# Optimization experiments

Hardware: AMD Instinct MI355X
Metric: run time of the kernel (lower is better)

Reference implementation:

```python
import jax, jax.numpy as jnp
import numpy as np

DIM = 1024
NPATCH = 256
NWINDOW = 8
HEADS = 16
DIM_HEAD = 64
T = NPATCH * NWINDOW  # 2048
B = 4


def setup_inputs() -> dict:
    key = jax.random.key(0)
    k1, k2, k3 = jax.random.split(key, 3)
    inner = HEADS * DIM_HEAD
    return {
        "x": jax.random.normal(k1, (B, T, DIM), dtype=jnp.float32),
        "ln_gamma": jnp.ones((DIM,), jnp.float32),
        "ln_beta": jnp.zeros((DIM,), jnp.float32),
        "w_qkv": jax.random.normal(k2, (DIM, 3 * inner), dtype=jnp.float32) * (DIM ** -0.5),
        "w_out": jax.random.normal(k3, (inner, DIM), dtype=jnp.float32) * (inner ** -0.5),
        "b_out": jnp.zeros((DIM,), jnp.float32),
    }


def reference(x, ln_gamma, ln_beta, w_qkv, w_out, b_out):
    Bq, Tq, C = x.shape
    # LayerNorm over last dim (eps matches torch default 1e-5)
    mu = jnp.mean(x, axis=-1, keepdims=True)
    var = jnp.mean(jnp.square(x - mu), axis=-1, keepdims=True)
    xn = (x - mu) * jax.lax.rsqrt(var + 1e-5) * ln_gamma + ln_beta
    # QKV projection (no bias), split heads: b t (h d) -> b h t d
    qkv = xn @ w_qkv  # [B, T, 3*H*D]
    q, k, v = jnp.split(qkv, 3, axis=-1)
    split_heads = lambda t: t.reshape(Bq, Tq, HEADS, DIM_HEAD).transpose(0, 2, 1, 3)
    q, k, v = split_heads(q), split_heads(k), split_heads(v)
    scale = DIM_HEAD ** -0.5
    dots = jnp.einsum("bhqd,bhkd->bhqk", q, k) * scale  # [B, H, T, T]
    # Block-causal mask: key block index <= query block index (block size = NPATCH)
    blk = jnp.arange(Tq) // NPATCH
    mask = blk[:, None] >= blk[None, :]  # [T, T] bool
    dots = jnp.where(mask, dots, jnp.float32(-jnp.inf))
    attn = jax.nn.softmax(dots, axis=-1)
    out = jnp.einsum("bhqk,bhkd->bhqd", attn, v)
    out = out.transpose(0, 2, 1, 3).reshape(Bq, Tq, HEADS * DIM_HEAD)
    return out @ w_out + b_out
```

## Files before the change

### kernel.cpp

```cpp
#include <hip/hip_runtime.h>
#include <hip/hip_bf16.h>
#include <stdint.h>

#define H_HEADS 16
#define D_HEAD  64
#define T_SEQ   2048
#define N_B     4
#define DIM_    1024
#define M_TOT   8192
#define N_QKV   3072

typedef unsigned short u16;
using f32x4  = __attribute__((ext_vector_type(4))) float;
using f32x16 = __attribute__((ext_vector_type(16))) float;
using bf16x8 = __attribute__((ext_vector_type(8))) short;

typedef __attribute__((address_space(3))) unsigned int lds_u32;
typedef __attribute__((address_space(1))) unsigned int glb_u32;

__device__ __forceinline__ void gload16(const u16* g, u16* l) {
  __builtin_amdgcn_global_load_lds((const glb_u32*)g, (lds_u32*)l, 16, 0, 0);
}

__device__ __forceinline__ u16 f2b(float f) {
  unsigned u = __builtin_bit_cast(unsigned, f);
  u += 0x7fffu + ((u >> 16) & 1u);
  return (u16)(u >> 16);
}

__global__ __launch_bounds__(256) void ln_kernel(const float* __restrict__ x,
    const float* __restrict__ gam, const float* __restrict__ bet,
    u16* __restrict__ xn)
{
  int row = blockIdx.x;
  int t = threadIdx.x;
  const float4* xr = (const float4*)(x + (size_t)row * DIM_);
  float4 v = xr[t];
  float s  = v.x + v.y + v.z + v.w;
  float s2 = v.x * v.x + v.y * v.y + v.z * v.z + v.w * v.w;
#pragma unroll
  for (int o = 32; o > 0; o >>= 1) { s += __shfl_down(s, o); s2 += __shfl_down(s2, o); }
  __shared__ float rs[4], rq[4];
  int w = t >> 6;
  if ((t & 63) == 0) { rs[w] = s; rq[w] = s2; }
  __syncthreads();
  float S  = rs[0] + rs[1] + rs[2] + rs[3];
  float S2 = rq[0] + rq[1] + rq[2] + rq[3];
  float mu   = S * (1.0f / DIM_);
  float var  = S2 * (1.0f / DIM_) - mu * mu;
  float rstd = rsqrtf(var + 1e-5f);
  float4 g4 = ((const float4*)gam)[t];
  float4 b4 = ((const float4*)bet)[t];
  ushort4 o;
  o.x = f2b((v.x - mu) * rstd * g4.x + b4.x);
  o.y = f2b((v.y - mu) * rstd * g4.y + b4.y);
  o.z = f2b((v.z - mu) * rstd * g4.z + b4.z);
  o.w = f2b((v.w - mu) * rstd * g4.w + b4.w);
  ((ushort4*)(xn + (size_t)row * DIM_))[t] = o;
}

__global__ __launch_bounds__(256) void transpose_cvt(const float* __restrict__ src,
    u16* __restrict__ dst, int K, int N)
{
  __shared__ u16 tile[32][33];
  int n0 = blockIdx.x * 32, k0 = blockIdx.y * 32;
  int tx = threadIdx.x, ty = threadIdx.y;
#pragma unroll
  for (int i = 0; i < 4; ++i) {
    int k = k0 + ty + i * 8;
    tile[tx][ty + i * 8] = f2b(src[(size_t)k * N + n0 + tx]);
  }
  __syncthreads();
#pragma unroll
  for (int i = 0; i < 4; ++i) {
    int n = n0 + ty + i * 8;
    dst[(size_t)n * K + k0 + tx] = tile[ty + i * 8][tx];
  }
}

template<int EPI>
__global__ __launch_bounds__(256) void gemm_bt(
    const u16* __restrict__ A, const u16* __restrict__ Bt, int K,
    u16* __restrict__ Qb, u16* __restrict__ Kb, u16* __restrict__ Vt,
    const float* __restrict__ bias, float* __restrict__ outF)
{
  __shared__ __align__(16) u16 lA[128 * 32];
  __shared__ __align__(16) u16 lB[128 * 32];
  int tid = threadIdx.x;
  int bn = blockIdx.x * 128, bm = blockIdx.y * 128;
  int lane = tid & 63, w = tid >> 6;
  int wr = w >> 1, wc = w & 1;
  int g = lane >> 4, r16 = lane & 15;
  const f32x4 fzero = {0.f, 0.f, 0.f, 0.f};
  f32x4 acc[4][4];
#pragma unroll
  for (int i = 0; i < 4; ++i)
#pragma unroll
    for (int j = 0; j < 4; ++j) acc[i][j] = fzero;

  const u16* Ab = A + (size_t)bm * K;
  const u16* Bb = Bt + (size_t)bn * K;

  for (int kt = 0; kt < K; kt += 32) {
    __syncthreads();
#pragma unroll
    for (int it = 0; it < 2; ++it) {
      int c = tid + it * 256;
      int row = c >> 2;
      int sc = (c & 3) ^ (row & 3);
      gload16(Ab + (size_t)row * K + kt + sc * 8, lA + c * 8);
      gload16(Bb + (size_t)row * K + kt + sc * 8, lB + c * 8);
    }
    __syncthreads();
    bf16x8 af[4], bf[4];
#pragma unroll
    for (int i = 0; i < 4; ++i) {
      int rl = wr * 64 + i * 16 + r16;
      af[i] = *(const bf16x8*)(lA + rl * 32 + ((g ^ (rl & 3)) << 3));
    }
#pragma unroll
    for (int j = 0; j < 4; ++j) {
      int rl = wc * 64 + j * 16 + r16;
      bf[j] = *(const bf16x8*)(lB + rl * 32 + ((g ^ (rl & 3)) << 3));
    }
#pragma unroll
    for (int i = 0; i < 4; ++i)
#pragma unroll
      for (int j = 0; j < 4; ++j)
        acc[i][j] = __builtin_amdgcn_mfma_f32_16x16x32_bf16(af[i], bf[j], acc[i][j], 0, 0, 0);
  }

  if (EPI == 0) {
    int part = bn >> 10;
#pragma unroll
    for (int i = 0; i < 4; ++i) {
#pragma unroll
      for (int j = 0; j < 4; ++j) {
        int n = bn + wc * 64 + j * 16 + r16;
        int nn = n & 1023;
        int h = nn >> 6, d = nn & 63;
#pragma unroll
        for (int rr = 0; rr < 4; ++rr) {
          int m = bm + wr * 64 + i * 16 + g * 4 + rr;
          int b = m >> 11, t = m & 2047;
          size_t bh = (size_t)(b * H_HEADS + h);
          float vv = acc[i][j][rr];
          if (part == 0)      Qb[(bh * T_SEQ + t) * D_HEAD + d] = f2b(vv * 0.18033688f);
          else if (part == 1) Kb[(bh * T_SEQ + t) * D_HEAD + d] = f2b(vv);
          else                Vt[(bh * D_HEAD + d) * T_SEQ + t] = f2b(vv);
        }
      }
    }
  } else {
#pragma unroll
    for (int i = 0; i < 4; ++i) {
#pragma unroll
      for (int j = 0; j < 4; ++j) {
        int n = bn + wc * 64 + j * 16 + r16;
        float bb = bias[n];
#pragma unroll
        for (int rr = 0; rr < 4; ++rr) {
          int m = bm + wr * 64 + i * 16 + g * 4 + rr;
          outF[(size_t)m * DIM_ + n] = acc[i][j][rr] + bb;
        }
      }
    }
  }
}

__global__ __launch_bounds__(512, 4) void attn_kernel(
    const u16* __restrict__ Qb, const u16* __restrict__ Kb,
    const u16* __restrict__ Vt, u16* __restrict__ AO)
{
  __shared__ __align__(16) u16 lK[2][64 * 64];
  __shared__ __align__(16) u16 lV[2][64 * 64];
  int bid = blockIdx.x;
  int bh6 = bid & 63;
  int h = bh6 & 15, b = bh6 >> 4;
  const int PERM[8] = {7, 5, 3, 1, 0, 2, 4, 6};
  int qt = PERM[bid >> 6];
  int nkt = (qt + 1) * 4;
  int tid = threadIdx.x, lane = tid & 63, w = tid >> 6;
  int q5 = lane & 31, hi = lane >> 5;
  size_t bh = (size_t)bh6;
  const u16* Qg = Qb + (bh * T_SEQ + (size_t)qt * 256) * D_HEAD;
  const u16* Kg = Kb + bh * T_SEQ * D_HEAD;
  const u16* Vg = Vt + bh * (size_t)D_HEAD * T_SEQ;

  bf16x8 qf[4];
#pragma unroll
  for (int kd = 0; kd < 4; ++kd)
    qf[kd] = *(const bf16x8*)(Qg + (w * 32 + q5) * D_HEAD + kd * 16 + hi * 8);

  f32x16 o0 = {0}, o1 = {0};
  float m_ = -1e30f, l_ = 0.f;

  auto STAGE = [&](int bs, int kt) {
    int c = tid;
    int row = c >> 3;
    int sc = (c & 7) ^ (row & 7);
    gload16(Kg + ((size_t)(kt * 64 + row)) * D_HEAD + sc * 8, &lK[bs][c * 8]);
    gload16(Vg + (size_t)row * T_SEQ + kt * 64 + sc * 8, &lV[bs][c * 8]);
  };

  STAGE(0, 0);
  int cur = 0;
  for (int kt = 0; kt < nkt; ++kt) {
    if (kt + 1 < nkt) {
      STAGE(cur ^ 1, kt + 1);
      asm volatile("s_waitcnt vmcnt(2)" ::: "memory");
    } else {
      asm volatile("s_waitcnt vmcnt(0)" ::: "memory");
    }
    __builtin_amdgcn_sched_barrier(0);
    __builtin_amdgcn_s_barrier();
    const u16* Kl = lK[cur];
    const u16* Vl = lV[cur];

    f32x16 s0 = {0}, s1 = {0};
    __builtin_amdgcn_s_setprio(1);
#pragma unroll
    for (int kd = 0; kd < 4; ++kd) {
      int ch = 2 * kd + hi;
      bf16x8 a0 = *(const bf16x8*)(Kl + q5 * 64 + ((ch ^ (q5 & 7)) << 3));
      bf16x8 a1 = *(const bf16x8*)(Kl + (32 + q5) * 64 + ((ch ^ (q5 & 7)) << 3));
      s0 = __builtin_amdgcn_mfma_f32_32x32x16_bf16(a0, qf[kd], s0, 0, 0, 0);
      s1 = __builtin_amdgcn_mfma_f32_32x32x16_bf16(a1, qf[kd], s1, 0, 0, 0);
    }
    __builtin_amdgcn_s_setprio(0);

    float pmax = fmaxf(s0[0], s1[0]);
#pragma unroll
    for (int r = 1; r < 16; ++r) pmax = fmaxf(pmax, fmaxf(s0[r], s1[r]));
    pmax = fmaxf(pmax, __shfl_xor(pmax, 32));
    float mnew = fmaxf(m_, pmax);
    float al = exp2f(m_ - mnew);
    m_ = mnew;
    float rsum = 0.f;
#pragma unroll
    for (int r = 0; r < 16; ++r) { s0[r] = exp2f(s0[r] - mnew); rsum += s0[r]; }
#pragma unroll
    for (int r = 0; r < 16; ++r) { s1[r] = exp2f(s1[r] - mnew); rsum += s1[r]; }
    rsum += __shfl_xor(rsum, 32);
    l_ = l_ * al + rsum;
    o0 *= al; o1 *= al;

    __builtin_amdgcn_s_setprio(1);
#pragma unroll
    for (int ks = 0; ks < 4; ++ks) {
      float v0 = (ks < 2) ? s0[(ks & 1) * 8 + 0] : s1[(ks & 1) * 8 + 0];
      float v1 = (ks < 2) ? s0[(ks & 1) * 8 + 1] : s1[(ks & 1) * 8 + 1];
      float v2 = (ks < 2) ? s0[(ks & 1) * 8 + 2] : s1[(ks & 1) * 8 + 2];
      float v3 = (ks < 2) ? s0[(ks & 1) * 8 + 3] : s1[(ks & 1) * 8 + 3];
      float v4 = (ks < 2) ? s0[(ks & 1) * 8 + 4] : s1[(ks & 1) * 8 + 4];
      float v5 = (ks < 2) ? s0[(ks & 1) * 8 + 5] : s1[(ks & 1) * 8 + 5];
      float v6 = (ks < 2) ? s0[(ks & 1) * 8 + 6] : s1[(ks & 1) * 8 + 6];
      float v7 = (ks < 2) ? s0[(ks & 1) * 8 + 7] : s1[(ks & 1) * 8 + 7];
      unsigned E0, E1, E2, E3;
      asm("v_cvt_pk_bf16_f32 %0, %1, %2" : "=v"(E0) : "v"(v0), "v"(v1));
      asm("v_cvt_pk_bf16_f32 %0, %1, %2" : "=v"(E1) : "v"(v2), "v"(v3));
      asm("v_cvt_pk_bf16_f32 %0, %1, %2" : "=v"(E2) : "v"(v4), "v"(v5));
      asm("v_cvt_pk_bf16_f32 %0, %1, %2" : "=v"(E3) : "v"(v6), "v"(v7));
      asm("v_permlane32_swap_b32 %0, %1" : "+v"(E0), "+v"(E2));
      asm("v_permlane32_swap_b32 %0, %1" : "+v"(E1), "+v"(E3));
      union { unsigned u[4]; bf16x8 v; } pk_;
      pk_.u[0] = E0; pk_.u[1] = E1; pk_.u[2] = E2; pk_.u[3] = E3;
      int ch = 2 * ks + hi;
      bf16x8 vf0 = *(const bf16x8*)(Vl + q5 * 64 + ((ch ^ (q5 & 7)) << 3));
      bf16x8 vf1 = *(const bf16x8*)(Vl + (32 + q5) * 64 + ((ch ^ (q5 & 7)) << 3));
      o0 = __builtin_amdgcn_mfma_f32_32x32x16_bf16(vf0, pk_.v, o0, 0, 0, 0);
      o1 = __builtin_amdgcn_mfma_f32_32x32x16_bf16(vf1, pk_.v, o1, 0, 0, 0);
    }
    __builtin_amdgcn_s_setprio(0);

    asm volatile("s_waitcnt lgkmcnt(0)" ::: "memory");
    __builtin_amdgcn_s_barrier();
    cur ^= 1;
  }

  float inv = 1.0f / l_;
  int t = qt * 256 + w * 32 + q5;
  u16* Ao = AO + ((size_t)b * T_SEQ + t) * DIM_ + h * 64;
#pragma unroll
  for (int rq = 0; rq < 4; ++rq) {
    ushort4 pk0, pk1;
    pk0.x = f2b(o0[rq * 4 + 0] * inv); pk0.y = f2b(o0[rq * 4 + 1] * inv);
    pk0.z = f2b(o0[rq * 4 + 2] * inv); pk0.w = f2b(o0[rq * 4 + 3] * inv);
    pk1.x = f2b(o1[rq * 4 + 0] * inv); pk1.y = f2b(o1[rq * 4 + 1] * inv);
    pk1.z = f2b(o1[rq * 4 + 2] * inv); pk1.w = f2b(o1[rq * 4 + 3] * inv);
    *(ushort4*)(Ao + rq * 8 + hi * 4)      = pk0;
    *(ushort4*)(Ao + 32 + rq * 8 + hi * 4) = pk1;
  }
}

extern "C" void kernel_launch(void* const* d_in, const int* in_sizes, int n_in,
                              void* d_out, int out_size, void* d_ws, size_t ws_size,
                              hipStream_t stream)
{
  const float* x    = (const float*)d_in[0];
  const float* gam  = (const float*)d_in[1];
  const float* bet  = (const float*)d_in[2];
  const float* wqkv = (const float*)d_in[3];
  const float* wout = (const float*)d_in[4];
  const float* bout = (const float*)d_in[5];
  float* out = (float*)d_out;

  u16* ws    = (u16*)d_ws;
  u16* xn    = ws;
  u16* wqkvT = xn    + (size_t)M_TOT * DIM_;
  u16* woutT = wqkvT + (size_t)N_QKV * DIM_;
  u16* Qb    = woutT + (size_t)DIM_ * DIM_;
  u16* Kb    = Qb    + (size_t)64 * T_SEQ * D_HEAD;
  u16* Vt    = Kb    + (size_t)64 * T_SEQ * D_HEAD;
  u16* AO    = xn;

  ln_kernel<<<M_TOT, 256, 0, stream>>>(x, gam, bet, xn);
  transpose_cvt<<<dim3(N_QKV / 32, DIM_ / 32), dim3(32, 8), 0, stream>>>(wqkv, wqkvT, DIM_, N_QKV);
  transpose_cvt<<<dim3(DIM_ / 32, DIM_ / 32), dim3(32, 8), 0, stream>>>(wout, woutT, DIM_, DIM_);
  gemm_bt<0><<<dim3(N_QKV / 128, M_TOT / 128), 256, 0, stream>>>(xn, wqkvT, DIM_, Qb, Kb, Vt, nullptr, nullptr);
  attn_kernel<<<N_B * H_HEADS * 8, 512, 0, stream>>>(Qb, Kb, Vt, AO);
  gemm_bt<1><<<dim3(DIM_ / 128, M_TOT / 128), 256, 0, stream>>>(AO, woutT, DIM_, nullptr, nullptr, nullptr, bout, out);
}
```

Baseline: 303.4 us.

## Rewrite projection GEMMs with 256x256 double-buffered tiles and 32x32 MFMA

Replaces the 128x128 single-buffered GEMM with a 512-thread kernel that computes 256x256 output tiles over a 64-wide K step. It uses 32x32x16 bf16 MFMA and double-buffers global-to-LDS loads so the next tile loads while the current one computes. It also maps blocks to XCDs for L2 locality and packs the V-transpose stores into 4-element vector writes. The aim is more data reuse per LDS byte and hidden load latency. In exchange, the 128KB LDS footprint allows only one block per CU, and the output projection launches just 128 blocks, which can leave CUs idle.

```diff
diff --git a/kernel.cpp b/kernel.cpp
--- a/kernel.cpp
+++ b/kernel.cpp
@@ -79,91 +79,137 @@
 }
 
 template<int EPI>
-__global__ __launch_bounds__(256) void gemm_bt(
-    const u16* __restrict__ A, const u16* __restrict__ Bt, int K,
+__global__ __launch_bounds__(512, 2) void gemm8(
+    const u16* __restrict__ A, const u16* __restrict__ Bt,
     u16* __restrict__ Qb, u16* __restrict__ Kb, u16* __restrict__ Vt,
     const float* __restrict__ bias, float* __restrict__ outF)
 {
-  __shared__ __align__(16) u16 lA[128 * 32];
-  __shared__ __align__(16) u16 lB[128 * 32];
-  int tid = threadIdx.x;
-  int bn = blockIdx.x * 128, bm = blockIdx.y * 128;
-  int lane = tid & 63, w = tid >> 6;
-  int wr = w >> 1, wc = w & 1;
-  int g = lane >> 4, r16 = lane & 15;
-  const f32x4 fzero = {0.f, 0.f, 0.f, 0.f};
-  f32x4 acc[4][4];
-#pragma unroll
-  for (int i = 0; i < 4; ++i)
-#pragma unroll
-    for (int j = 0; j < 4; ++j) acc[i][j] = fzero;
-
-  const u16* Ab = A + (size_t)bm * K;
-  const u16* Bb = Bt + (size_t)bn * K;
-
-  for (int kt = 0; kt < K; kt += 32) {
-    __syncthreads();
-#pragma unroll
-    for (int it = 0; it < 2; ++it) {
-      int c = tid + it * 256;
-      int row = c >> 2;
-      int sc = (c & 3) ^ (row & 3);
-      gload16(Ab + (size_t)row * K + kt + sc * 8, lA + c * 8);
-      gload16(Bb + (size_t)row * K + kt + sc * 8, lB + c * 8);
-    }
-    __syncthreads();
-    bf16x8 af[4], bf[4];
-#pragma unroll
-    for (int i = 0; i < 4; ++i) {
-      int rl = wr * 64 + i * 16 + r16;
-      af[i] = *(const bf16x8*)(lA + rl * 32 + ((g ^ (rl & 3)) << 3));
-    }
-#pragma unroll
-    for (int j = 0; j < 4; ++j) {
-      int rl = wc * 64 + j * 16 + r16;
-      bf[j] = *(const bf16x8*)(lB + rl * 32 + ((g ^ (rl & 3)) << 3));
-    }
-#pragma unroll
-    for (int i = 0; i < 4; ++i)
-#pragma unroll
-      for (int j = 0; j < 4; ++j)
-        acc[i][j] = __builtin_amdgcn_mfma_f32_16x16x32_bf16(af[i], bf[j], acc[i][j], 0, 0, 0);
+  __shared__ __align__(16) u16 lds[2][512 * 64];
+  const int tid = threadIdx.x;
+  const int lane = tid & 63, w = tid >> 6;
+  const int wr = w >> 2, wc = w & 3;
+  const int c5 = lane & 31, hi = lane >> 5;
+
+  int bid = blockIdx.x;
+  int xcd = bid & 7, i = bid >> 3;
+  int bm = (xcd * 4 + (i & 3)) * 256;
+  int bn = (i >> 2) * 256;
+
+  const u16* Ag = A  + (size_t)bm * 1024;
+  const u16* Bg = Bt + (size_t)bn * 1024;
+
+  f32x16 acc[4][2];
+#pragma unroll
+  for (int rf = 0; rf < 4; ++rf)
+#pragma unroll
+    for (int cf = 0; cf < 2; ++cf) acc[rf][cf] = (f32x16){0};
+
+  auto STAGE = [&](int bs, int kt) {
+    int rr = tid >> 3, cc = tid & 7;
+#pragma unroll
+    for (int r = 0; r < 4; ++r) {
+      int row = r * 64 + rr;
+      int sc = cc ^ (row & 7);
+      gload16(Ag + (size_t)row * 1024 + kt * 64 + sc * 8, &lds[bs][row * 64 + cc * 8]);
+    }
+#pragma unroll
+    for (int r = 0; r < 4; ++r) {
+      int row = r * 64 + rr;
+      int sc = cc ^ (row & 7);
+      gload16(Bg + (size_t)row * 1024 + kt * 64 + sc * 8, &lds[bs][(256 + row) * 64 + cc * 8]);
+    }
+  };
+
+  STAGE(0, 0);
+  asm volatile("s_waitcnt vmcnt(0)" ::: "memory");
+  __builtin_amdgcn_s_barrier();
+
+  for (int kt = 0; kt < 16; ++kt) {
+    int ct = kt & 1;
+    if (kt + 1 < 16) STAGE(ct ^ 1, kt + 1);
+    const u16* lA = &lds[ct][(wr * 128) * 64];
+    const u16* lB = &lds[ct][(256 + wc * 64) * 64];
+    int sw = c5 & 7;
+
+    bf16x8 bfr[2][4];
+#pragma unroll
+    for (int cf = 0; cf < 2; ++cf)
+#pragma unroll
+      for (int ks = 0; ks < 4; ++ks)
+        bfr[cf][ks] = *(const bf16x8*)(lB + (cf * 32 + c5) * 64 + (((ks * 2 + hi) ^ sw) * 8));
+
+#pragma unroll
+    for (int rh = 0; rh < 2; ++rh) {
+      bf16x8 afr[2][4];
+#pragma unroll
+      for (int f = 0; f < 2; ++f)
+#pragma unroll
+        for (int ks = 0; ks < 4; ++ks)
+          afr[f][ks] = *(const bf16x8*)(lA + ((rh * 2 + f) * 32 + c5) * 64 + (((ks * 2 + hi) ^ sw) * 8));
+#pragma unroll
+      for (int cf = 0; cf < 2; ++cf) {
+        __builtin_amdgcn_s_setprio(1);
+#pragma unroll
+        for (int f = 0; f < 2; ++f)
+#pragma unroll
+          for (int ks = 0; ks < 4; ++ks)
+            acc[rh * 2 + f][cf] = __builtin_amdgcn_mfma_f32_32x32x16_bf16(
+                afr[f][ks], bfr[cf][ks], acc[rh * 2 + f][cf], 0, 0, 0);
+        __builtin_amdgcn_s_setprio(0);
+      }
+    }
+
+    asm volatile("s_waitcnt vmcnt(0)" ::: "memory");
+    __builtin_amdgcn_sched_barrier(0);
+    __builtin_amdgcn_s_barrier();
   }
 
   if (EPI == 0) {
     int part = bn >> 10;
 #pragma unroll
-    for (int i = 0; i < 4; ++i) {
-#pragma unroll
-      for (int j = 0; j < 4; ++j) {
-        int n = bn + wc * 64 + j * 16 + r16;
+    for (int rf = 0; rf < 4; ++rf) {
+#pragma unroll
+      for (int cf = 0; cf < 2; ++cf) {
+        int n = bn + wc * 64 + cf * 32 + c5;
         int nn = n & 1023;
         int h = nn >> 6, d = nn & 63;
 #pragma unroll
-        for (int rr = 0; rr < 4; ++rr) {
-          int m = bm + wr * 64 + i * 16 + g * 4 + rr;
-          int b = m >> 11, t = m & 2047;
+        for (int q = 0; q < 4; ++q) {
+          int mb = bm + wr * 128 + rf * 32 + 8 * q + 4 * hi;
+          int b = mb >> 11, t0 = mb & 2047;
           size_t bh = (size_t)(b * H_HEADS + h);
-          float vv = acc[i][j][rr];
-          if (part == 0)      Qb[(bh * T_SEQ + t) * D_HEAD + d] = f2b(vv * 0.18033688f);
-          else if (part == 1) Kb[(bh * T_SEQ + t) * D_HEAD + d] = f2b(vv);
-          else                Vt[(bh * D_HEAD + d) * T_SEQ + t] = f2b(vv);
+          if (part == 2) {
+            ushort4 pk;
+            pk.x = f2b(acc[rf][cf][q * 4 + 0]); pk.y = f2b(acc[rf][cf][q * 4 + 1]);
+            pk.z = f2b(acc[rf][cf][q * 4 + 2]); pk.w = f2b(acc[rf][cf][q * 4 + 3]);
+            *(ushort4*)(Vt + (bh * D_HEAD + d) * T_SEQ + t0) = pk;
+          } else {
+#pragma unroll
+            for (int e = 0; e < 4; ++e) {
+              float vv = acc[rf][cf][q * 4 + e];
+              if (part == 0)
+                Qb[(bh * T_SEQ + t0 + e) * D_HEAD + d] = f2b(vv * 0.18033688f);
+              else
+                Kb[(bh * T_SEQ + t0 + e) * D_HEAD + d] = f2b(vv);
+            }
+          }
         }
       }
     }
   } else {
 #pragma unroll
-    for (int i = 0; i < 4; ++i) {
-#pragma unroll
-      for (int j = 0; j < 4; ++j) {
-        int n = bn + wc * 64 + j * 16 + r16;
-        float bb = bias[n];
-#pragma unroll
-        for (int rr = 0; rr < 4; ++rr) {
-          int m = bm + wr * 64 + i * 16 + g * 4 + rr;
-          outF[(size_t)m * DIM_ + n] = acc[i][j][rr] + bb;
+    for (int cf = 0; cf < 2; ++cf) {
+      int n = bn + wc * 64 + cf * 32 + c5;
+      float bb = bias[n];
+#pragma unroll
+      for (int rf = 0; rf < 4; ++rf)
+#pragma unroll
+        for (int q = 0; q < 4; ++q) {
+          int mb = bm + wr * 128 + rf * 32 + 8 * q + 4 * hi;
+#pragma unroll
+          for (int e = 0; e < 4; ++e)
+            outF[(size_t)(mb + e) * DIM_ + n] = acc[rf][cf][q * 4 + e] + bb;
         }
-      }
     }
   }
 }
@@ -317,7 +363,7 @@
   ln_kernel<<<M_TOT, 256, 0, stream>>>(x, gam, bet, xn);
   transpose_cvt<<<dim3(N_QKV / 32, DIM_ / 32), dim3(32, 8), 0, stream>>>(wqkv, wqkvT, DIM_, N_QKV);
   transpose_cvt<<<dim3(DIM_ / 32, DIM_ / 32), dim3(32, 8), 0, stream>>>(wout, woutT, DIM_, DIM_);
-  gemm_bt<0><<<dim3(N_QKV / 128, M_TOT / 128), 256, 0, stream>>>(xn, wqkvT, DIM_, Qb, Kb, Vt, nullptr, nullptr);
+  gemm8<0><<<(M_TOT / 256) * (N_QKV / 256), 512, 0, stream>>>(xn, wqkvT, Qb, Kb, Vt, nullptr, nullptr);
   attn_kernel<<<N_B * H_HEADS * 8, 512, 0, stream>>>(Qb, Kb, Vt, AO);
-  gemm_bt<1><<<dim3(DIM_ / 128, M_TOT / 128), 256, 0, stream>>>(AO, woutT, DIM_, nullptr, nullptr, nullptr, bout, out);
-}
+  gemm8<1><<<(M_TOT / 256) * (DIM_ / 256), 512, 0, stream>>>(AO, woutT, nullptr, nullptr, nullptr, bout, out);
+}
```

Result: faster. 289.2 us (-4.7%).
